# Performance work log

Measured on AMD Instinct MI355X. Metric: run time of the kernel, lower is better.

The kernel has to match this reference:

```python
import jax, jax.numpy as jnp
import numpy as np

D = 50          # half-window
K = 2 * D + 1   # 101 window positions
P_SIZE = 100    # predictive-alignment hidden dim


def setup_inputs() -> dict:
    key = jax.random.key(0)
    ks = jax.random.split(key, 5)
    B, S, CQ, CC = 2, 2048, 256, 256
    q = jax.random.normal(ks[0], (B, S, CQ), jnp.float32)
    c_t = jax.random.normal(ks[1], (B, S, CC), jnp.float32)
    W_a = jax.random.normal(ks[2], (CC, CQ), jnp.float32) / np.sqrt(CQ).astype(np.float32)
    W_p = jax.random.normal(ks[3], (P_SIZE, CC), jnp.float32) / np.sqrt(CC).astype(np.float32)
    V_p = jax.random.normal(ks[4], (1, P_SIZE), jnp.float32) / np.sqrt(P_SIZE).astype(np.float32)
    return {"q": q, "c_t": c_t, "W_a": W_a, "W_p": W_p, "V_p": V_p}


def reference(q, c_t, W_a, W_p, V_p):
    B, S, CQ = q.shape
    # predictive alignment: p in (0, S), one predicted center per (b, s)
    p = S * jax.nn.sigmoid(jnp.tanh(c_t @ W_p.T) @ V_p.T)[..., 0]          # [B,S]
    offs = jnp.arange(-D, D + 1)                                           # [K]
    # torch .long() truncates toward zero (raw can be negative)
    raw = jnp.trunc(p[..., None] + offs[None, None, :] + 1.0).astype(jnp.int32)
    # clamp to [0, S+1] then mod (S+1): index 0 == padded (invalid) row,
    # matching torch's NaN-padded row 0 (S+1 wraps to 0 via the modulo)
    idx = jnp.clip(raw, 0, S + 1) % (S + 1)                                # [B,S,K]
    mask = idx == 0                                                        # invalid window slots
    # pad row 0 (torch pads with NaN then zeroes the NaN rows; we pad with 0
    # and mask by index -> identical math for finite q)
    q_pad = jnp.concatenate([jnp.zeros((B, 1, CQ), q.dtype), q], axis=1)   # [B,S+1,CQ]
    gathered = jnp.take_along_axis(q_pad, idx.reshape(B, S * K, 1), axis=1)
    q1 = jnp.where(mask[..., None], 0.0, gathered.reshape(B, S, K, CQ))    # [B,S,K,CQ]
    # score: W_a projection then dot with context
    Wq = jnp.einsum("bskq,cq->bskc", q1, W_a)                              # [B,S,K,CC]
    a = jnp.einsum("bskc,bsc->bsk", Wq, c_t)                               # [B,S,K]
    a = jnp.where(mask, -jnp.inf, a)
    attn = jax.nn.softmax(a, axis=2)                                       # [B,S,K]
    # gaussian decay centered at floor(p) (p > 0 so trunc == floor)
    exponent = -2.0 * (((offs[None, None, :] + jnp.trunc(p)[..., None] - p[..., None]) / D) ** 2)
    w = attn * jnp.exp(exponent)                                           # [B,S,K]
    s_t = jnp.einsum("bsk,bskc->bsc", w, q1)                               # [B,S,CQ]
    return s_t
```

## Files before the change

kernel.cpp:

```cpp
#include <hip/hip_runtime.h>
#include <math.h>

#define S_LEN 2048
#define NB    2
#define CQ_   256
#define CC_   256
#define DH    50
#define KW    101
#define PS    100
#define RB    4
#define HPAD  128

__global__ __launch_bounds__(128) void k_prep(const float* __restrict__ Wp,
                                              float* __restrict__ WpT) {
  const int c = blockIdx.x, j = threadIdx.x;
  WpT[c * HPAD + j] = (j < PS) ? Wp[j * CC_ + c] : 0.0f;
}

__global__ __launch_bounds__(384) void k_align(const float* __restrict__ ct,
    const float* __restrict__ Wa, const float* __restrict__ WpT,
    const float* __restrict__ Vp, float* __restrict__ p_out,
    float* __restrict__ V_out) {
  const int r0  = blockIdx.x * RB;
  const int tid = threadIdx.x;

  __shared__ float sc[RB][CC_];
  {
    const float4* src = (const float4*)(ct + (size_t)r0 * CC_);
    float4* dst = (float4*)&sc[0][0];
    if (tid < RB * CC_ / 4) dst[tid] = src[tid];
  }
  __syncthreads();

  const float* wp;
  int w1s;
  if (tid < CQ_) { wp = Wa + tid;          w1s = CQ_;  }
  else           { wp = WpT + (tid - CQ_); w1s = HPAD; }
  const int w2s = 2 * w1s, w3s = 3 * w1s, w4s = 4 * w1s;

  float acc[RB];
#pragma unroll
  for (int r = 0; r < RB; ++r) acc[r] = 0.0f;

#pragma unroll 2
  for (int c = 0; c < CC_; c += 4) {
    const float w0 = wp[0];
    const float w1 = wp[w1s];
    const float w2 = wp[w2s];
    const float w3 = wp[w3s];
#pragma unroll
    for (int r = 0; r < RB; ++r) {
      const float4 cv = *(const float4*)&sc[r][c];
      float t = acc[r];
      t = fmaf(cv.x, w0, t);
      t = fmaf(cv.y, w1, t);
      t = fmaf(cv.z, w2, t);
      t = fmaf(cv.w, w3, t);
      acc[r] = t;
    }
    wp += w4s;
  }

  if (tid < CQ_) {
#pragma unroll
    for (int r = 0; r < RB; ++r)
      V_out[(size_t)(r0 + r) * CQ_ + tid] = acc[r];
  }

  __shared__ float red[RB][PS + 4];
  if (tid >= CQ_ && tid < CQ_ + PS) {
    const int j = tid - CQ_;
    const float vp = Vp[j];
#pragma unroll
    for (int r = 0; r < RB; ++r) red[r][j] = vp * tanhf(acc[r]);
  }
  __syncthreads();
  if (tid < RB) {
    float s = 0.0f;
    for (int j = 0; j < PS; ++j) s += red[tid][j];
    p_out[r0 + tid] = (float)S_LEN * (1.0f / (1.0f + expf(-s)));
  }
}

__global__ __launch_bounds__(256) void k_attn(const float* __restrict__ q,
    const float* __restrict__ p_in, const float* V,
    float* out) {
  const int wid  = threadIdx.x >> 6;
  const int row  = (blockIdx.x << 2) + wid;
  const int lane = threadIdx.x & 63;
  const int b    = row >> 11;

  __shared__ float ss[4][128];
  __shared__ float sw[4][128];

  const float p  = p_in[row];
  const float tp = truncf(p);
  const float* qb = q + (size_t)b * S_LEN * CQ_;

  const int sub = lane >> 4;
  const int cb  = (lane & 15) * 16;

  const float* vrow = V + (size_t)row * CQ_ + cb;
  const float4 v0 = *(const float4*)(vrow);
  const float4 v1 = *(const float4*)(vrow + 4);
  const float4 v2 = *(const float4*)(vrow + 8);
  const float4 v3 = *(const float4*)(vrow + 12);

  if (lane >= KW - 64) ss[wid][64 + lane] = -INFINITY;

#pragma unroll 2
  for (int g = 0; g < 26; ++g) {
    const int k = (g << 2) + sub;
    const float t = p + (float)(k - DH) + 1.0f;
    const int raw = (int)t;
    const bool ok = (raw >= 1) && (raw <= S_LEN) && (k < KW);
    const int r = ok ? raw - 1 : 0;
    const float* qr = qb + (size_t)r * CQ_ + cb;
    const float4 q0 = *(const float4*)(qr);
    const float4 q1 = *(const float4*)(qr + 4);
    const float4 q2 = *(const float4*)(qr + 8);
    const float4 q3 = *(const float4*)(qr + 12);

    float s = q0.x * v0.x;
    s = fmaf(q0.y, v0.y, s);
    s = fmaf(q0.z, v0.z, s);
    s = fmaf(q0.w, v0.w, s);
    s = fmaf(q1.x, v1.x, s);
    s = fmaf(q1.y, v1.y, s);
    s = fmaf(q1.z, v1.z, s);
    s = fmaf(q1.w, v1.w, s);
    s = fmaf(q2.x, v2.x, s);
    s = fmaf(q2.y, v2.y, s);
    s = fmaf(q2.z, v2.z, s);
    s = fmaf(q2.w, v2.w, s);
    s = fmaf(q3.x, v3.x, s);
    s = fmaf(q3.y, v3.y, s);
    s = fmaf(q3.z, v3.z, s);
    s = fmaf(q3.w, v3.w, s);

    s += __shfl_xor(s, 1, 64);
    s += __shfl_xor(s, 2, 64);
    s += __shfl_xor(s, 4, 64);
    s += __shfl_xor(s, 8, 64);
    s = ok ? s : -INFINITY;
    if ((lane & 15) == 0) ss[wid][k] = s;
  }

  const float s0 = ss[wid][lane];
  const float s1 = ss[wid][64 + lane];

  float m = fmaxf(s0, s1);
#pragma unroll
  for (int off = 1; off < 64; off <<= 1) m = fmaxf(m, __shfl_xor(m, off, 64));

  const float e0 = __expf(s0 - m);
  const float e1 = __expf(s1 - m);
  float den = e0 + e1;
#pragma unroll
  for (int off = 1; off < 64; off <<= 1) den += __shfl_xor(den, off, 64);
  const float inv = 1.0f / den;

  float g0 = ((float)(lane - DH) + tp - p) / (float)DH;
  float g1 = ((float)(lane + (64 - DH)) + tp - p) / (float)DH;
  const float w0 = e0 * __expf(-2.0f * g0 * g0) * inv;
  const float w1 = e1 * __expf(-2.0f * g1 * g1) * inv;
  sw[wid][lane] = w0;
  if (lane < KW - 64) sw[wid][64 + lane] = w1;

  float4 acc = make_float4(0.0f, 0.0f, 0.0f, 0.0f);
  for (int k = 0; k < KW; ++k) {
    const float wk = sw[wid][k];
    if (wk > 1e-5f) {
      const float t = p + (float)(k - DH) + 1.0f;
      const int r   = (int)t - 1;
      const float4 qv = *(const float4*)(qb + (size_t)r * CQ_ + lane * 4);
      acc.x = fmaf(wk, qv.x, acc.x);
      acc.y = fmaf(wk, qv.y, acc.y);
      acc.z = fmaf(wk, qv.z, acc.z);
      acc.w = fmaf(wk, qv.w, acc.w);
    }
  }
  *(float4*)(out + (size_t)row * CQ_ + lane * 4) = acc;
}

extern "C" void kernel_launch(void* const* d_in, const int* in_sizes, int n_in,
                              void* d_out, int out_size, void* d_ws, size_t ws_size,
                              hipStream_t stream) {
  const float* q  = (const float*)d_in[0];
  const float* ct = (const float*)d_in[1];
  const float* Wa = (const float*)d_in[2];
  const float* Wp = (const float*)d_in[3];
  const float* Vp = (const float*)d_in[4];
  float* out = (float*)d_out;

  float* ws     = (float*)d_ws;
  float* p_ws   = ws;
  float* WpT_ws = ws + NB * S_LEN;

  k_prep <<<CC_, HPAD, 0, stream>>>(Wp, WpT_ws);
  k_align<<<(NB * S_LEN) / RB, 384, 0, stream>>>(ct, Wa, WpT_ws, Vp, p_ws, out);
  k_attn <<<(NB * S_LEN) / 4, 256, 0, stream>>>(q, p_ws, out, out);
}
```

Baseline: 128.1 us.

## Restructure align projection with register prefetch and ballot-compacted weighted gather

The alignment kernel now processes 8 rows per block and reads the context rows straight from global memory into registers with a software-prefetched double buffer, replacing the shared-memory staging and the barrier that preceded the loop. The Wa and Wp projection paths are split into separate branches. The attention kernel's score loop handles two window positions per iteration with split accumulators, and the weighted sum uses ballot masks to visit only window positions above the weight threshold, four gathers at a time, instead of scanning all 101 with a branch. Launch bounds now carry occupancy hints, which may limit registers and risk spills given the larger per-thread register arrays.

```diff
diff --git a/kernel.cpp b/kernel.cpp
--- a/kernel.cpp
+++ b/kernel.cpp
@@ -8,8 +8,9 @@
 #define DH    50
 #define KW    101
 #define PS    100
-#define RB    4
+#define RB    8
 #define HPAD  128
+#define WTH   1e-5f
 
 __global__ __launch_bounds__(128) void k_prep(const float* __restrict__ Wp,
                                               float* __restrict__ WpT) {
@@ -17,62 +18,107 @@
   WpT[c * HPAD + j] = (j < PS) ? Wp[j * CC_ + c] : 0.0f;
 }
 
-__global__ __launch_bounds__(384) void k_align(const float* __restrict__ ct,
+__global__ __launch_bounds__(384, 3) void k_align(const float* __restrict__ ct,
     const float* __restrict__ Wa, const float* __restrict__ WpT,
     const float* __restrict__ Vp, float* __restrict__ p_out,
     float* __restrict__ V_out) {
   const int r0  = blockIdx.x * RB;
   const int tid = threadIdx.x;
-
-  __shared__ float sc[RB][CC_];
-  {
-    const float4* src = (const float4*)(ct + (size_t)r0 * CC_);
-    float4* dst = (float4*)&sc[0][0];
-    if (tid < RB * CC_ / 4) dst[tid] = src[tid];
-  }
-  __syncthreads();
-
-  const float* wp;
-  int w1s;
-  if (tid < CQ_) { wp = Wa + tid;          w1s = CQ_;  }
-  else           { wp = WpT + (tid - CQ_); w1s = HPAD; }
-  const int w2s = 2 * w1s, w3s = 3 * w1s, w4s = 4 * w1s;
-
-  float acc[RB];
-#pragma unroll
-  for (int r = 0; r < RB; ++r) acc[r] = 0.0f;
-
-#pragma unroll 2
-  for (int c = 0; c < CC_; c += 4) {
-    const float w0 = wp[0];
-    const float w1 = wp[w1s];
-    const float w2 = wp[w2s];
-    const float w3 = wp[w3s];
+  const float* crow = ct + (size_t)r0 * CC_;
+
+  __shared__ float red[RB][PS + 4];
+
+  if (tid < CQ_) {
+    const float* wa = Wa + tid;
+    float acc[RB];
+#pragma unroll
+    for (int r = 0; r < RB; ++r) acc[r] = 0.0f;
+
+    float4 cv0[RB], cv1[RB];
+#pragma unroll
+    for (int r = 0; r < RB; ++r) cv0[r] = *(const float4*)&crow[r * CC_];
+    float w00 = wa[0 * CQ_], w01 = wa[1 * CQ_], w02 = wa[2 * CQ_], w03 = wa[3 * CQ_];
+
+    for (int c = 0; c < CC_ - 4; c += 4) {
+      const int cn = c + 4;
+#pragma unroll
+      for (int r = 0; r < RB; ++r) cv1[r] = *(const float4*)&crow[r * CC_ + cn];
+      const float w10 = wa[(size_t)(cn + 0) * CQ_];
+      const float w11 = wa[(size_t)(cn + 1) * CQ_];
+      const float w12 = wa[(size_t)(cn + 2) * CQ_];
+      const float w13 = wa[(size_t)(cn + 3) * CQ_];
+#pragma unroll
+      for (int r = 0; r < RB; ++r) {
+        float t = acc[r];
+        t = fmaf(cv0[r].x, w00, t);
+        t = fmaf(cv0[r].y, w01, t);
+        t = fmaf(cv0[r].z, w02, t);
+        t = fmaf(cv0[r].w, w03, t);
+        acc[r] = t;
+      }
+#pragma unroll
+      for (int r = 0; r < RB; ++r) cv0[r] = cv1[r];
+      w00 = w10; w01 = w11; w02 = w12; w03 = w13;
+    }
 #pragma unroll
     for (int r = 0; r < RB; ++r) {
-      const float4 cv = *(const float4*)&sc[r][c];
       float t = acc[r];
-      t = fmaf(cv.x, w0, t);
-      t = fmaf(cv.y, w1, t);
-      t = fmaf(cv.z, w2, t);
-      t = fmaf(cv.w, w3, t);
+      t = fmaf(cv0[r].x, w00, t);
+      t = fmaf(cv0[r].y, w01, t);
+      t = fmaf(cv0[r].z, w02, t);
+      t = fmaf(cv0[r].w, w03, t);
       acc[r] = t;
     }
-    wp += w4s;
-  }
-
-  if (tid < CQ_) {
 #pragma unroll
     for (int r = 0; r < RB; ++r)
       V_out[(size_t)(r0 + r) * CQ_ + tid] = acc[r];
-  }
-
-  __shared__ float red[RB][PS + 4];
-  if (tid >= CQ_ && tid < CQ_ + PS) {
+  } else {
     const int j = tid - CQ_;
-    const float vp = Vp[j];
-#pragma unroll
-    for (int r = 0; r < RB; ++r) red[r][j] = vp * tanhf(acc[r]);
+    const float* wh = WpT + j;
+    float ah[RB];
+#pragma unroll
+    for (int r = 0; r < RB; ++r) ah[r] = 0.0f;
+
+    float4 cv0[RB], cv1[RB];
+#pragma unroll
+    for (int r = 0; r < RB; ++r) cv0[r] = *(const float4*)&crow[r * CC_];
+    float w00 = wh[0 * HPAD], w01 = wh[1 * HPAD], w02 = wh[2 * HPAD], w03 = wh[3 * HPAD];
+
+    for (int c = 0; c < CC_ - 4; c += 4) {
+      const int cn = c + 4;
+#pragma unroll
+      for (int r = 0; r < RB; ++r) cv1[r] = *(const float4*)&crow[r * CC_ + cn];
+      const float w10 = wh[(size_t)(cn + 0) * HPAD];
+      const float w11 = wh[(size_t)(cn + 1) * HPAD];
+      const float w12 = wh[(size_t)(cn + 2) * HPAD];
+      const float w13 = wh[(size_t)(cn + 3) * HPAD];
+#pragma unroll
+      for (int r = 0; r < RB; ++r) {
+        float t = ah[r];
+        t = fmaf(cv0[r].x, w00, t);
+        t = fmaf(cv0[r].y, w01, t);
+        t = fmaf(cv0[r].z, w02, t);
+        t = fmaf(cv0[r].w, w03, t);
+        ah[r] = t;
+      }
+#pragma unroll
+      for (int r = 0; r < RB; ++r) cv0[r] = cv1[r];
+      w00 = w10; w01 = w11; w02 = w12; w03 = w13;
+    }
+#pragma unroll
+    for (int r = 0; r < RB; ++r) {
+      float t = ah[r];
+      t = fmaf(cv0[r].x, w00, t);
+      t = fmaf(cv0[r].y, w01, t);
+      t = fmaf(cv0[r].z, w02, t);
+      t = fmaf(cv0[r].w, w03, t);
+      ah[r] = t;
+    }
+    if (j < PS) {
+      const float vp = Vp[j];
+#pragma unroll
+      for (int r = 0; r < RB; ++r) red[r][j] = vp * tanhf(ah[r]);
+    }
   }
   __syncthreads();
   if (tid < RB) {
@@ -82,7 +128,7 @@
   }
 }
 
-__global__ __launch_bounds__(256) void k_attn(const float* __restrict__ q,
+__global__ __launch_bounds__(256, 4) void k_attn(const float* __restrict__ q,
     const float* __restrict__ p_in, const float* V,
     float* out) {
   const int wid  = threadIdx.x >> 6;
@@ -108,42 +154,56 @@
 
   if (lane >= KW - 64) ss[wid][64 + lane] = -INFINITY;
 
-#pragma unroll 2
-  for (int g = 0; g < 26; ++g) {
-    const int k = (g << 2) + sub;
-    const float t = p + (float)(k - DH) + 1.0f;
-    const int raw = (int)t;
-    const bool ok = (raw >= 1) && (raw <= S_LEN) && (k < KW);
-    const int r = ok ? raw - 1 : 0;
-    const float* qr = qb + (size_t)r * CQ_ + cb;
-    const float4 q0 = *(const float4*)(qr);
-    const float4 q1 = *(const float4*)(qr + 4);
-    const float4 q2 = *(const float4*)(qr + 8);
-    const float4 q3 = *(const float4*)(qr + 12);
-
-    float s = q0.x * v0.x;
-    s = fmaf(q0.y, v0.y, s);
-    s = fmaf(q0.z, v0.z, s);
-    s = fmaf(q0.w, v0.w, s);
-    s = fmaf(q1.x, v1.x, s);
-    s = fmaf(q1.y, v1.y, s);
-    s = fmaf(q1.z, v1.z, s);
-    s = fmaf(q1.w, v1.w, s);
-    s = fmaf(q2.x, v2.x, s);
-    s = fmaf(q2.y, v2.y, s);
-    s = fmaf(q2.z, v2.z, s);
-    s = fmaf(q2.w, v2.w, s);
-    s = fmaf(q3.x, v3.x, s);
-    s = fmaf(q3.y, v3.y, s);
-    s = fmaf(q3.z, v3.z, s);
-    s = fmaf(q3.w, v3.w, s);
-
-    s += __shfl_xor(s, 1, 64);
-    s += __shfl_xor(s, 2, 64);
-    s += __shfl_xor(s, 4, 64);
-    s += __shfl_xor(s, 8, 64);
-    s = ok ? s : -INFINITY;
-    if ((lane & 15) == 0) ss[wid][k] = s;
+  for (int g = 0; g < 26; g += 2) {
+    const int ka = (g << 2) + sub;
+    const int kb = ka + 4;
+    const float ta = p + (float)(ka - DH) + 1.0f;
+    const float tb = p + (float)(kb - DH) + 1.0f;
+    const int rawa = (int)ta;
+    const int rawb = (int)tb;
+    const bool oka = (rawa >= 1) && (rawa <= S_LEN) && (ka < KW);
+    const bool okb = (rawb >= 1) && (rawb <= S_LEN) && (kb < KW);
+    const float* qra = qb + (size_t)(oka ? rawa - 1 : 0) * CQ_ + cb;
+    const float* qrb = qb + (size_t)(okb ? rawb - 1 : 0) * CQ_ + cb;
+
+    const float4 a0 = *(const float4*)(qra);
+    const float4 a1 = *(const float4*)(qra + 4);
+    const float4 a2 = *(const float4*)(qra + 8);
+    const float4 a3 = *(const float4*)(qra + 12);
+    const float4 b0 = *(const float4*)(qrb);
+    const float4 b1 = *(const float4*)(qrb + 4);
+    const float4 b2 = *(const float4*)(qrb + 8);
+    const float4 b3 = *(const float4*)(qrb + 12);
+
+    float t0 = a0.x * v0.x, t1 = a1.x * v1.x, t2 = a2.x * v2.x, t3 = a3.x * v3.x;
+    t0 = fmaf(a0.y, v0.y, t0); t1 = fmaf(a1.y, v1.y, t1);
+    t2 = fmaf(a2.y, v2.y, t2); t3 = fmaf(a3.y, v3.y, t3);
+    t0 = fmaf(a0.z, v0.z, t0); t1 = fmaf(a1.z, v1.z, t1);
+    t2 = fmaf(a2.z, v2.z, t2); t3 = fmaf(a3.z, v3.z, t3);
+    t0 = fmaf(a0.w, v0.w, t0); t1 = fmaf(a1.w, v1.w, t1);
+    t2 = fmaf(a2.w, v2.w, t2); t3 = fmaf(a3.w, v3.w, t3);
+    float sA = (t0 + t1) + (t2 + t3);
+    sA += __shfl_xor(sA, 1, 64);
+    sA += __shfl_xor(sA, 2, 64);
+    sA += __shfl_xor(sA, 4, 64);
+    sA += __shfl_xor(sA, 8, 64);
+    sA = oka ? sA : -INFINITY;
+    if ((lane & 15) == 0) ss[wid][ka] = sA;
+
+    float u0 = b0.x * v0.x, u1 = b1.x * v1.x, u2 = b2.x * v2.x, u3 = b3.x * v3.x;
+    u0 = fmaf(b0.y, v0.y, u0); u1 = fmaf(b1.y, v1.y, u1);
+    u2 = fmaf(b2.y, v2.y, u2); u3 = fmaf(b3.y, v3.y, u3);
+    u0 = fmaf(b0.z, v0.z, u0); u1 = fmaf(b1.z, v1.z, u1);
+    u2 = fmaf(b2.z, v2.z, u2); u3 = fmaf(b3.z, v3.z, u3);
+    u0 = fmaf(b0.w, v0.w, u0); u1 = fmaf(b1.w, v1.w, u1);
+    u2 = fmaf(b2.w, v2.w, u2); u3 = fmaf(b3.w, v3.w, u3);
+    float sB = (u0 + u1) + (u2 + u3);
+    sB += __shfl_xor(sB, 1, 64);
+    sB += __shfl_xor(sB, 2, 64);
+    sB += __shfl_xor(sB, 4, 64);
+    sB += __shfl_xor(sB, 8, 64);
+    sB = okb ? sB : -INFINITY;
+    if ((lane & 15) == 0) ss[wid][kb] = sB;
   }
 
   const float s0 = ss[wid][lane];
@@ -167,17 +227,31 @@
   sw[wid][lane] = w0;
   if (lane < KW - 64) sw[wid][64 + lane] = w1;
 
+  unsigned long long m0 = __ballot(w0 > WTH);
+  unsigned long long m1 = __ballot((lane < KW - 64) && (w1 > WTH));
+
   float4 acc = make_float4(0.0f, 0.0f, 0.0f, 0.0f);
-  for (int k = 0; k < KW; ++k) {
-    const float wk = sw[wid][k];
-    if (wk > 1e-5f) {
-      const float t = p + (float)(k - DH) + 1.0f;
-      const int r   = (int)t - 1;
-      const float4 qv = *(const float4*)(qb + (size_t)r * CQ_ + lane * 4);
-      acc.x = fmaf(wk, qv.x, acc.x);
-      acc.y = fmaf(wk, qv.y, acc.y);
-      acc.z = fmaf(wk, qv.z, acc.z);
-      acc.w = fmaf(wk, qv.w, acc.w);
+  while ((m0 | m1) != 0ull) {
+    int kk[4];
+#pragma unroll
+    for (int i = 0; i < 4; ++i) {
+      int k = -1;
+      if (m0)      { k = __builtin_ctzll(m0);      m0 &= m0 - 1; }
+      else if (m1) { k = 64 + __builtin_ctzll(m1); m1 &= m1 - 1; }
+      kk[i] = k;
+    }
+#pragma unroll
+    for (int i = 0; i < 4; ++i) {
+      if (kk[i] >= 0) {
+        const float wk = sw[wid][kk[i]];
+        const float t = p + (float)(kk[i] - DH) + 1.0f;
+        const int r = (int)t - 1;
+        const float4 qv = *(const float4*)(qb + (size_t)r * CQ_ + lane * 4);
+        acc.x = fmaf(wk, qv.x, acc.x);
+        acc.y = fmaf(wk, qv.y, acc.y);
+        acc.z = fmaf(wk, qv.z, acc.z);
+        acc.w = fmaf(wk, qv.w, acc.w);
+      }
     }
   }
   *(float4*)(out + (size_t)row * CQ_ + lane * 4) = acc;
```

New measurement: 120.1 us. -6.3%, faster.
